# Kernel optimization log

Measured on AMD Instinct MI355X. Metric: run time of the kernel, lower is better.

Reference implementation:

```python
import jax, jax.numpy as jnp
import numpy as np

COST_KEYPOINT = 1.0
COST_GIOU = 1.0


def box_cxcyczwhd_to_xyzxyz(b):
    c, s = b[..., :3], b[..., 3:]
    return jnp.concatenate([c - 0.5 * s, c + 0.5 * s], axis=-1)


def generalized_3d_box_iou(b1, b2):
    # b1: [N,6], b2: [M,6], both xyzxyz. Returns [N,M] GIoU.
    vol1 = jnp.prod(b1[:, 3:] - b1[:, :3], axis=-1)
    vol2 = jnp.prod(b2[:, 3:] - b2[:, :3], axis=-1)
    lt = jnp.maximum(b1[:, None, :3], b2[None, :, :3])
    rb = jnp.minimum(b1[:, None, 3:], b2[None, :, 3:])
    inter = jnp.prod(jnp.maximum(rb - lt, 0.0), axis=-1)
    union = vol1[:, None] + vol2[None, :] - inter
    iou = inter / union
    elt = jnp.minimum(b1[:, None, :3], b2[None, :, :3])
    erb = jnp.maximum(b1[:, None, 3:], b2[None, :, 3:])
    evol = jnp.prod(jnp.maximum(erb - elt, 0.0), axis=-1)
    return iou - (evol - union) / evol


@jax.jit
def compute_cost(pred_keypoints, pred_boxes, tgt_boxes, tgt_keypoints):
    bs, Q = pred_keypoints.shape[:2]
    out_kp = pred_keypoints.reshape(bs * Q, -1)            # [bs*Q, K*3]
    out_boxes = pred_boxes.reshape(bs * Q, 6)
    tgt_b = tgt_boxes.reshape(-1, 6)                        # [T_total, 6]
    tgt_kp = tgt_keypoints.reshape(tgt_b.shape[0], -1)      # [T_total, K*3]
    xyz_min = box_cxcyczwhd_to_xyzxyz(tgt_b)[:, :3]
    K3 = tgt_kp.shape[-1]
    kp = tgt_kp.reshape(-1, K3 // 3, 3)
    # normalize keypoints relative to box min-corner and box size
    dist_kp = ((kp - xyz_min[:, None, :]) / tgt_b[:, None, 3:]).reshape(-1, K3)
    # L1 cdist: [bs*Q, T_total]
    cost_kp = jnp.sum(jnp.abs(out_kp[:, None, :] - dist_kp[None, :, :]), axis=-1)
    cost_giou = -generalized_3d_box_iou(
        box_cxcyczwhd_to_xyzxyz(out_boxes), box_cxcyczwhd_to_xyzxyz(tgt_b))
    C = COST_KEYPOINT * cost_kp + COST_GIOU * cost_giou
    return C.reshape(bs, Q, -1)


def _lap(cost):
    # Jonker-Volgenant shortest-augmenting-path LAP (scipy-style).
    # cost: [n, m] with n <= m. Returns (arange(n), col4row).
    cost = np.asarray(cost, dtype=np.float64)
    n, m = cost.shape
    u = np.zeros(n)
    v = np.zeros(m)
    col4row = np.full(n, -1, np.int64)
    row4col = np.full(m, -1, np.int64)
    for curRow in range(n):
        path = np.full(m, -1, np.int64)
        SR = np.zeros(n, bool)
        SC = np.zeros(m, bool)
        shortest = np.full(m, np.inf)
        minVal = 0.0
        i = curRow
        sink = -1
        while sink == -1:
            SR[i] = True
            idx = np.where(~SC)[0]
            r = minVal + cost[i, idx] - u[i] - v[idx]
            better = r < shortest[idx]
            shortest[idx[better]] = r[better]
            path[idx[better]] = i
            jloc = np.argmin(shortest[idx])
            j = idx[jloc]
            minVal = shortest[j]
            SC[j] = True
            if row4col[j] == -1:
                sink = j
            else:
                i = row4col[j]
        u[curRow] += minVal
        mask = SR.copy()
        mask[curRow] = False
        u[mask] += minVal - shortest[col4row[mask]]
        v[SC] -= minVal - shortest[SC]
        j = sink
        while True:
            i = path[j]
            row4col[j] = i
            col4row[i], j = j, col4row[i]
            if i == curRow:
                break
    return np.arange(n), col4row


def _linear_sum_assignment(cost):
    # cost: [Q, T] with Q >= T; mirrors scipy's transpose handling:
    # returns (row_ind sorted ascending, matching col_ind).
    rows, cols = _lap(cost.T)  # rows = arange(T) targets, cols = query ids
    order = np.argsort(cols)
    return cols[order], rows[order]


def setup_inputs() -> dict:
    key = jax.random.key(0)
    k1, k2, k3, k4, k5, k6 = jax.random.split(key, 6)
    BS, Q, T, K = 16, 300, 50, 17
    pred_keypoints = jax.random.normal(k1, (BS, Q, K * 3), dtype=jnp.float32)
    pred_boxes = jnp.concatenate([
        jax.random.uniform(k2, (BS, Q, 3), dtype=jnp.float32),
        jax.random.uniform(k3, (BS, Q, 3), dtype=jnp.float32) * 0.5 + 0.05,
    ], axis=-1)
    tgt_boxes = jnp.concatenate([
        jax.random.uniform(k4, (BS, T, 3), dtype=jnp.float32),
        jax.random.uniform(k5, (BS, T, 3), dtype=jnp.float32) * 0.5 + 0.05,
    ], axis=-1)
    tgt_keypoints = jax.random.uniform(k6, (BS, T, K * 3), dtype=jnp.float32)
    return {"pred_keypoints": pred_keypoints, "pred_boxes": pred_boxes,
            "tgt_boxes": tgt_boxes, "tgt_keypoints": tgt_keypoints}


def reference(pred_keypoints, pred_boxes, tgt_boxes, tgt_keypoints):
    C = compute_cost(pred_keypoints, pred_boxes, tgt_boxes, tgt_keypoints)
    Cn = np.asarray(C)
    bs, Q, _ = Cn.shape
    T = tgt_boxes.shape[1]
    # per-image block of the column-split cost matrix, as in torch C.split(sizes, -1)
    idx = []
    for b in range(bs):
        i, j = _linear_sum_assignment(Cn[b, :, b * T:(b + 1) * T])
        idx.append(np.stack([i, j]))
    indices = jnp.asarray(np.stack(idx), dtype=jnp.int32)  # [bs, 2, T]
    return C, indices
```

## Files before the change

### kernel.cpp

```cpp
#include <hip/hip_runtime.h>
#include <math.h>

#define BSZ 16
#define NQ 300
#define NT 50
#define K3 51
#define NPRED (BSZ*NQ)
#define NTGT  (BSZ*NT)
#define NC    (NPRED*NTGT)
#define TSTRIDE 301
#define SMEMF 15232

template<int CTRL, int RMASK>
__device__ __forceinline__ double dpp_minstep_f64(double x) {
    long long bb = __double_as_longlong(x);
    int lo = (int)(bb & 0xFFFFFFFFll);
    int hi = (int)(bb >> 32);
    int mlo = __builtin_amdgcn_update_dpp(lo, lo, CTRL, RMASK, 0xF, false);
    int mhi = __builtin_amdgcn_update_dpp(hi, hi, CTRL, RMASK, 0xF, false);
    double other = __longlong_as_double(((long long)mhi << 32) | (long long)(unsigned)mlo);
    return fmin(x, other);
}
__device__ __forceinline__ double wave_min_f64(double x) {
    x = dpp_minstep_f64<0xB1, 0xF>(x);
    x = dpp_minstep_f64<0x4E, 0xF>(x);
    x = dpp_minstep_f64<0x141, 0xF>(x);
    x = dpp_minstep_f64<0x140, 0xF>(x);
    x = dpp_minstep_f64<0x142, 0xA>(x);
    x = dpp_minstep_f64<0x143, 0xC>(x);
    long long bb = __double_as_longlong(x);
    int lo = __builtin_amdgcn_readlane((int)(bb & 0xFFFFFFFFll), 63);
    int hi = __builtin_amdgcn_readlane((int)(bb >> 32), 63);
    return __longlong_as_double(((long long)hi << 32) | (long long)(unsigned)lo);
}
__device__ __forceinline__ double readlane_f64(double x, int lane) {
    long long bb = __double_as_longlong(x);
    int lo = __builtin_amdgcn_readlane((int)(bb & 0xFFFFFFFFll), lane);
    int hi = __builtin_amdgcn_readlane((int)(bb >> 32), lane);
    return __longlong_as_double(((long long)hi << 32) | (long long)(unsigned)lo);
}

__device__ __forceinline__ float giou_cost(
    float plt0, float plt1, float plt2, float prb0, float prb1, float prb2, float pvol,
    float tlt0, float tlt1, float tlt2, float trb0, float trb1, float trb2, float tvol)
{
    float inter = fmaxf(fminf(prb0,trb0) - fmaxf(plt0,tlt0), 0.f);
    inter *= fmaxf(fminf(prb1,trb1) - fmaxf(plt1,tlt1), 0.f);
    inter *= fmaxf(fminf(prb2,trb2) - fmaxf(plt2,tlt2), 0.f);
    float evol = fmaxf(fmaxf(prb0,trb0) - fminf(plt0,tlt0), 0.f);
    evol *= fmaxf(fmaxf(prb1,trb1) - fminf(plt1,tlt1), 0.f);
    evol *= fmaxf(fmaxf(prb2,trb2) - fminf(plt2,tlt2), 0.f);
    float uni = pvol + tvol - inter;
    return inter/uni - (evol - uni)/evol;
}

__global__ __launch_bounds__(1024) void fused_kernel(
    const float* __restrict__ pred_kp, const float* __restrict__ pred_boxes,
    const float* __restrict__ tgt_boxes, const float* __restrict__ tgt_kp,
    float* __restrict__ C, float* __restrict__ out_idx)
{
    __shared__ __align__(16) float smem[SMEMF];
    const int bid = blockIdx.x;
    const int tid = threadIdx.x;

    if (bid >= BSZ) {
        const int cb = bid - BSZ;
        const int pb = cb % 75, tb = cb / 75;
        const int p0 = pb * 64, t0 = tb * 80;
        float* s_dk   = smem;
        float* s_tbox = smem + 4480;
        float* s_pk   = smem + 5440;

        if (tid < 80) {
            const float* tb6 = tgt_boxes + (size_t)(t0 + tid) * 6;
            float c0=tb6[0], c1=tb6[1], c2=tb6[2], s0=tb6[3], s1=tb6[4], s2=tb6[5];
            float l0=c0-0.5f*s0, l1=c1-0.5f*s1, l2=c2-0.5f*s2;
            float r0=c0+0.5f*s0, r1=c1+0.5f*s1, r2=c2+0.5f*s2;
            float* tw = s_tbox + tid*12;
            tw[0]=l0; tw[1]=l1; tw[2]=l2; tw[3]=r0; tw[4]=r1; tw[5]=r2;
            tw[6]=(r0-l0)*(r1-l1)*(r2-l2);
            tw[9]=s0; tw[10]=s1; tw[11]=s2;
        }
        __syncthreads();
        for (int e = tid; e < 80*K3; e += 1024) {
            int t = e / K3; int c = e - t*K3; int d = c % 3;
            float kp = tgt_kp[(size_t)t0*K3 + e];
            s_dk[t*56 + c] = (kp - s_tbox[t*12 + d]) / s_tbox[t*12 + 9 + d];
        }
        for (int e = tid; e < 64*K3; e += 1024)
            s_pk[e] = pred_kp[(size_t)p0*K3 + e];
        __syncthreads();

        const int pl = tid & 63, g = tid >> 6;
        float a[K3];
        #pragma unroll
        for (int c = 0; c < K3; ++c) a[c] = s_pk[pl*K3 + c];
        const int p = p0 + pl;
        const float* pb6 = pred_boxes + (size_t)p * 6;
        float pc0=pb6[0],pc1=pb6[1],pc2=pb6[2],ps0=pb6[3],ps1=pb6[4],ps2=pb6[5];
        float plt0=pc0-0.5f*ps0, plt1=pc1-0.5f*ps1, plt2=pc2-0.5f*ps2;
        float prb0=pc0+0.5f*ps0, prb1=pc1+0.5f*ps1, prb2=pc2+0.5f*ps2;
        float pvol=(prb0-plt0)*(prb1-plt1)*(prb2-plt2);

        #pragma unroll
        for (int k = 0; k < 5; ++k) {
            int tl = g*5 + k;
            const float* bbp = s_dk + tl*56;
            float sum = 0.f;
            #pragma unroll
            for (int c4 = 0; c4 < 12; ++c4) {
                float4 q = *(const float4*)(bbp + 4*c4);
                sum += fabsf(a[4*c4+0] - q.x);
                sum += fabsf(a[4*c4+1] - q.y);
                sum += fabsf(a[4*c4+2] - q.z);
                sum += fabsf(a[4*c4+3] - q.w);
            }
            sum += fabsf(a[48] - bbp[48]);
            sum += fabsf(a[49] - bbp[49]);
            sum += fabsf(a[50] - bbp[50]);
            const float* tw = s_tbox + tl*12;
            float g_ = giou_cost(plt0,plt1,plt2,prb0,prb1,prb2,pvol,
                                 tw[0],tw[1],tw[2],tw[3],tw[4],tw[5],tw[6]);
            C[(size_t)p*NTGT + (t0+tl)] = sum - g_;
        }
        return;
    }

    const int b = bid;
    const int ln = tid & 63, w = tid >> 6;
    const int bq0 = b*NQ, bt0 = b*NT;
    float* tile = smem;

    for (int e = tid; e < NT*K3; e += 1024)
        tile[e] = tgt_kp[(size_t)bt0*K3 + e];
    __syncthreads();

    float dk[K3];
    float tl0=0,tl1=0,tl2=0,tr0=0,tr1=0,tr2=0,tvol=0;
    if (ln < NT) {
        const float* tb6 = tgt_boxes + (size_t)(bt0+ln)*6;
        float c0=tb6[0],c1=tb6[1],c2=tb6[2],s0=tb6[3],s1=tb6[4],s2=tb6[5];
        tl0=c0-0.5f*s0; tl1=c1-0.5f*s1; tl2=c2-0.5f*s2;
        tr0=c0+0.5f*s0; tr1=c1+0.5f*s1; tr2=c2+0.5f*s2;
        tvol=(tr0-tl0)*(tr1-tl1)*(tr2-tl2);
        #pragma unroll
        for (int c = 0; c < K3; ++c) {
            int d = c % 3;
            float L = (d==0)?tl0:((d==1)?tl1:tl2);
            float S = (d==0)?s0:((d==1)?s1:s2);
            dk[c] = (tile[ln*K3 + c] - L) / S;
        }
    }
    __syncthreads();

    for (int p = w; p < NQ; p += 16) {
        const float* prow = pred_kp + (size_t)(bq0+p)*K3;
        const float* pb6  = pred_boxes + (size_t)(bq0+p)*6;
        float pc0=pb6[0],pc1=pb6[1],pc2=pb6[2],ps0=pb6[3],ps1=pb6[4],ps2=pb6[5];
        float plt0=pc0-0.5f*ps0, plt1=pc1-0.5f*ps1, plt2=pc2-0.5f*ps2;
        float prb0=pc0+0.5f*ps0, prb1=pc1+0.5f*ps1, prb2=pc2+0.5f*ps2;
        float pvol=(prb0-plt0)*(prb1-plt1)*(prb2-plt2);
        if (ln < NT) {
            float sum = 0.f;
            #pragma unroll
            for (int c = 0; c < K3; ++c) sum += fabsf(prow[c] - dk[c]);
            float g_ = giou_cost(plt0,plt1,plt2,prb0,prb1,prb2,pvol,
                                 tl0,tl1,tl2,tr0,tr1,tr2,tvol);
            tile[ln*TSTRIDE + p] = sum - g_;
        }
    }
    __syncthreads();

    float* s_rmv = smem + 15072;
    int*   s_rmc = (int*)(smem + 15136);
    for (int r = w; r < NT; r += 16) {
        float bv = __builtin_inff(); int bj = 0x7fffffff;
        #pragma unroll
        for (int s = 0; s < 5; ++s) {
            int j = ln + 64*s;
            if (j < NQ) {
                float cv = tile[r*TSTRIDE + j];
                if (cv < bv || (cv == bv && j < bj)) { bv = cv; bj = j; }
            }
        }
        #pragma unroll
        for (int off = 32; off > 0; off >>= 1) {
            float ov = __shfl_xor(bv, off);
            int   oj = __shfl_xor(bj, off);
            if (ov < bv || (ov == bv && oj < bj)) { bv = ov; bj = oj; }
        }
        if (ln == 0) { s_rmv[r] = bv; s_rmc[r] = bj; }
    }
    __syncthreads();
    if (w != 0) return;

    double u = 0.0;
    int c4r = -1;
    if (ln < NT) u = (double)s_rmv[ln];
    int wantj = (ln < NT) ? s_rmc[ln] : -1;
    for (int r = 0; r < NT; ++r) {
        int j = __builtin_amdgcn_readlane(wantj, r);
        unsigned long long taken = __ballot((ln < NT) && (c4r == j));
        if (taken == 0ull && ln == r) c4r = j;
    }

    double v[5], sh[5];
    int pth[5];
    #pragma unroll
    for (int s = 0; s < 5; ++s) v[s] = 0.0;
    const double DINF = __builtin_inf();

    for (int curRow = 0; curRow < NT; ++curRow) {
        if (__builtin_amdgcn_readlane(c4r, curRow) >= 0) continue;
        #pragma unroll
        for (int s = 0; s < 5; ++s) { sh[s] = DINF; pth[s] = -1; }
        int SCm = (ln < 44) ? 0 : 0x10;
        unsigned long long SRmask = 0ull;
        int i = curRow;
        double minVal = 0.0;
        int sink = -1;

        while (true) {
            SRmask |= (1ull << i);
            float cf[5];
            #pragma unroll
            for (int s = 0; s < 5; ++s) cf[s] = tile[i*TSTRIDE + ln + 64*s];
            double u_i = readlane_f64(u, i);
            double lmin = DINF;
            #pragma unroll
            for (int s = 0; s < 5; ++s) {
                bool open = ((SCm >> s) & 1) == 0;
                double r = ((minVal + (double)cf[s]) - u_i) - v[s];
                bool upd = open && (r < sh[s]);
                sh[s]  = upd ? r : sh[s];
                pth[s] = upd ? i : pth[s];
                lmin = fmin(lmin, open ? sh[s] : DINF);
            }
            double m = wave_min_f64(lmin);
            minVal = m;
            unsigned long long b0 = __ballot((((SCm >> 0) & 1) == 0) && (sh[0] == m));
            unsigned long long b1 = __ballot((((SCm >> 1) & 1) == 0) && (sh[1] == m));
            unsigned long long b2 = __ballot((((SCm >> 2) & 1) == 0) && (sh[2] == m));
            unsigned long long b3 = __ballot((((SCm >> 3) & 1) == 0) && (sh[3] == m));
            unsigned long long b4 = __ballot((((SCm >> 4) & 1) == 0) && (sh[4] == m));
            int jstar;
            if      (b0) jstar =       __builtin_ctzll(b0);
            else if (b1) jstar =  64 + __builtin_ctzll(b1);
            else if (b2) jstar = 128 + __builtin_ctzll(b2);
            else if (b3) jstar = 192 + __builtin_ctzll(b3);
            else         jstar = 256 + __builtin_ctzll(b4);
            if (ln == (jstar & 63)) SCm |= 1 << (jstar >> 6);
            unsigned long long mm = __ballot((ln < NT) && (c4r == jstar));
            if (mm == 0ull) { sink = jstar; break; }
            i = __builtin_ctzll(mm);
        }

        int cg  = (c4r >= 0) ? c4r : 0;
        int gow = cg & 63, gsl = cg >> 6;
        double g0 = __shfl(sh[0], gow);
        double g1 = __shfl(sh[1], gow);
        double g2 = __shfl(sh[2], gow);
        double g3 = __shfl(sh[3], gow);
        double g4 = __shfl(sh[4], gow);
        double gg = g0;
        gg = (gsl == 1) ? g1 : gg;
        gg = (gsl == 2) ? g2 : gg;
        gg = (gsl == 3) ? g3 : gg;
        gg = (gsl == 4) ? g4 : gg;
        bool inSR = (ln < NT) && ((SRmask >> ln) & 1ull);
        double du = (ln == curRow) ? minVal : (minVal - gg);
        u = inSR ? (u + du) : u;
        #pragma unroll
        for (int s = 0; s < 5; ++s) {
            bool closed = ((SCm >> s) & 1) != 0;
            v[s] = closed ? (v[s] - (minVal - sh[s])) : v[s];
        }

        int j = sink;
        while (true) {
            int ow2 = j & 63, sl2 = j >> 6;
            int ps = pth[0];
            ps = (sl2==1) ? pth[1] : ps;
            ps = (sl2==2) ? pth[2] : ps;
            ps = (sl2==3) ? pth[3] : ps;
            ps = (sl2==4) ? pth[4] : ps;
            int ii = __builtin_amdgcn_readlane(ps, ow2);
            int jj = __builtin_amdgcn_readlane(c4r, ii);
            if (ln == ii) c4r = j;
            j = jj;
            if (ii == curRow) break;
        }
    }

    int* smem_i = (int*)smem;
    __threadfence_block();
    if (ln < NT) smem_i[ln] = c4r;
    __threadfence_block();
    int myc = c4r;
    int rank = 0;
    for (int s2 = 0; s2 < NT; ++s2) rank += (smem_i[s2] < myc) ? 1 : 0;
    if (ln < NT) {
        out_idx[b*(2*NT) + rank]      = (float)myc;
        out_idx[b*(2*NT) + NT + rank] = (float)ln;
    }
}

extern "C" void kernel_launch(void* const* d_in, const int* in_sizes, int n_in,
                              void* d_out, int out_size, void* d_ws, size_t ws_size,
                              hipStream_t stream)
{
    const float* pred_kp    = (const float*)d_in[0];
    const float* pred_boxes = (const float*)d_in[1];
    const float* tgt_boxes  = (const float*)d_in[2];
    const float* tgt_kp     = (const float*)d_in[3];
    float* C   = (float*)d_out;
    float* idx = C + NC;
    fused_kernel<<<dim3(BSZ + 750), 1024, 0, stream>>>(
        pred_kp, pred_boxes, tgt_boxes, tgt_kp, C, idx);
}
```

Before: 130.3 us.

## Restructure JV augmentation to track only matched columns plus per-row unmatched minima

Rewrites the shortest-augmenting-path LAP so each lane tracks one matched column slot instead of five column slots per lane. Unmatched columns have v=0, so their reduced cost is given by each row's cheapest unmatched column. Those minima come from a precomputed per-row sorted top-12 list in shared memory, with a full-row rescan when the list runs out. This cuts per-iteration work from five slots and five ballots to one, at the cost of an extra top-k precompute phase and more complex bookkeeping that could diverge on ties.

```diff
diff --git a/kernel.cpp b/kernel.cpp
--- a/kernel.cpp
+++ b/kernel.cpp
@@ -9,7 +9,15 @@
 #define NTGT  (BSZ*NT)
 #define NC    (NPRED*NTGT)
 #define TSTRIDE 301
-#define SMEMF 15232
+#define LT 12
+#define SMEMF 16176
+
+#define OFF_RMV 15072
+#define OFF_RMC 15136
+#define OFF_LV  15200
+#define OFF_LC  15800
+#define OFF_MB  16100
+
 
 template<int CTRL, int RMASK>
 __device__ __forceinline__ double dpp_minstep_f64(double x) {
@@ -38,6 +46,23 @@
     int lo = __builtin_amdgcn_readlane((int)(bb & 0xFFFFFFFFll), lane);
     int hi = __builtin_amdgcn_readlane((int)(bb >> 32), lane);
     return __longlong_as_double(((long long)hi << 32) | (long long)(unsigned)lo);
+}
+__device__ __forceinline__ float readlane_f32(float x, int lane) {
+    return __int_as_float(__builtin_amdgcn_readlane(__float_as_int(x), lane));
+}
+__device__ __forceinline__ double shfl_f64(double x, int lane) {
+    long long bb = __double_as_longlong(x);
+    int lo = __shfl((int)(bb & 0xFFFFFFFFll), lane);
+    int hi = __shfl((int)(bb >> 32), lane);
+    return __longlong_as_double(((long long)hi << 32) | (long long)(unsigned)lo);
+}
+__device__ __forceinline__ void wave_argmin_f32(float &bv, int &bj) {
+    #pragma unroll
+    for (int off = 32; off > 0; off >>= 1) {
+        float ov = __shfl_xor(bv, off);
+        int   oj = __shfl_xor(bj, off);
+        if (ov < bv || (ov == bv && oj < bj)) { bv = ov; bj = oj; }
+    }
 }
 
 __device__ __forceinline__ float giou_cost(
@@ -171,8 +196,12 @@
     }
     __syncthreads();
 
-    float* s_rmv = smem + 15072;
-    int*   s_rmc = (int*)(smem + 15136);
+    float* s_rmv = smem + OFF_RMV;
+    int*   s_rmc = (int*)(smem + OFF_RMC);
+    float* s_lv  = smem + OFF_LV;
+    unsigned short* s_lc = (unsigned short*)(smem + OFF_LC);
+    unsigned char*  s_mb = (unsigned char*)(smem + OFF_MB);
+
     for (int r = w; r < NT; r += 16) {
         float bv = __builtin_inff(); int bj = 0x7fffffff;
         #pragma unroll
@@ -183,14 +212,30 @@
                 if (cv < bv || (cv == bv && j < bj)) { bv = cv; bj = j; }
             }
         }
-        #pragma unroll
-        for (int off = 32; off > 0; off >>= 1) {
-            float ov = __shfl_xor(bv, off);
-            int   oj = __shfl_xor(bj, off);
-            if (ov < bv || (ov == bv && oj < bj)) { bv = ov; bj = oj; }
-        }
+        wave_argmin_f32(bv, bj);
         if (ln == 0) { s_rmv[r] = bv; s_rmc[r] = bj; }
     }
+    for (int r = w; r < NT; r += 16) {
+        float v5[5]; int excl = 0;
+        #pragma unroll
+        for (int s = 0; s < 5; ++s) {
+            int j = ln + 64*s;
+            v5[s] = (j < NQ) ? tile[r*TSTRIDE + j] : __builtin_inff();
+        }
+        for (int k = 0; k < LT; ++k) {
+            float bv = __builtin_inff(); int bj = 0x7fffffff;
+            #pragma unroll
+            for (int s = 0; s < 5; ++s) {
+                int j = ln + 64*s;
+                bool ok = (j < NQ) && !((excl >> s) & 1);
+                if (ok && (v5[s] < bv || (v5[s] == bv && j < bj))) { bv = v5[s]; bj = j; }
+            }
+            wave_argmin_f32(bv, bj);
+            if (ln == 0) { s_lv[r*LT + k] = bv; s_lc[r*LT + k] = (unsigned short)bj; }
+            if (ln == (bj & 63)) excl |= 1 << (bj >> 6);
+        }
+    }
+    for (int e = tid; e < 76; e += 1024) ((int*)(smem + OFF_MB))[e] = 0;
     __syncthreads();
     if (w != 0) return;
 
@@ -203,92 +248,119 @@
         unsigned long long taken = __ballot((ln < NT) && (c4r == j));
         if (taken == 0ull && ln == r) c4r = j;
     }
-
-    double v[5], sh[5];
-    int pth[5];
-    #pragma unroll
-    for (int s = 0; s < 5; ++s) v[s] = 0.0;
+    if (ln < NT && c4r >= 0) s_mb[c4r] = 1;
+    __threadfence_block();
+
+    float buval = __builtin_inff(); int bucol = 0x7fffffff; int buptr = LT;
+    if (ln < NT) {
+        buptr = 0;
+        while (buptr < LT && s_mb[s_lc[ln*LT + buptr]]) ++buptr;
+        if (buptr < LT) { buval = s_lv[ln*LT + buptr]; bucol = s_lc[ln*LT + buptr]; }
+    }
+    {
+        unsigned long long rs = __ballot((ln < NT) && (buptr >= LT));
+        while (rs) {
+            int r = __builtin_ctzll(rs); rs &= rs - 1;
+            float bv = __builtin_inff(); int bj = 0x7fffffff;
+            #pragma unroll
+            for (int s = 0; s < 5; ++s) {
+                int j = ln + 64*s;
+                if (j < NQ && !s_mb[j]) {
+                    float cv = tile[r*TSTRIDE + j];
+                    if (cv < bv || (cv == bv && j < bj)) { bv = cv; bj = j; }
+                }
+            }
+            wave_argmin_f32(bv, bj);
+            if (ln == r) { buval = bv; bucol = bj; }
+        }
+    }
+
+    int nm = 0;
+    int mcol = 0, mrow = 0, s4r = 0;
+    double vs = 0.0;
+    for (int r = 0; r < NT; ++r) {
+        int cr = __builtin_amdgcn_readlane(c4r, r);
+        if (cr >= 0) {
+            if (ln == nm) { mcol = cr; mrow = r; }
+            if (ln == r) s4r = nm;
+            ++nm;
+        }
+    }
+
     const double DINF = __builtin_inf();
 
     for (int curRow = 0; curRow < NT; ++curRow) {
         if (__builtin_amdgcn_readlane(c4r, curRow) >= 0) continue;
-        #pragma unroll
-        for (int s = 0; s < 5; ++s) { sh[s] = DINF; pth[s] = -1; }
-        int SCm = (ln < 44) ? 0 : 0x10;
+        bool open = (ln < nm);
+        double sh = DINF; int pthr = -1;
         unsigned long long SRmask = 0ull;
         int i = curRow;
         double minVal = 0.0;
-        int sink = -1;
-
-        while (true) {
+        double sinkCand = DINF; int sinkCol = -1, sinkRow = -1;
+
+        for (int guard = 0; guard < 512; ++guard) {
             SRmask |= (1ull << i);
-            float cf[5];
-            #pragma unroll
-            for (int s = 0; s < 5; ++s) cf[s] = tile[i*TSTRIDE + ln + 64*s];
-            double u_i = readlane_f64(u, i);
-            double lmin = DINF;
-            #pragma unroll
-            for (int s = 0; s < 5; ++s) {
-                bool open = ((SCm >> s) & 1) == 0;
-                double r = ((minVal + (double)cf[s]) - u_i) - v[s];
-                bool upd = open && (r < sh[s]);
-                sh[s]  = upd ? r : sh[s];
-                pth[s] = upd ? i : pth[s];
-                lmin = fmin(lmin, open ? sh[s] : DINF);
-            }
-            double m = wave_min_f64(lmin);
+            float cf = tile[i*TSTRIDE + mcol];
+            double u_i  = readlane_f64(u, i);
+            float  bu_i = readlane_f32(buval, i);
+            int    buc_i = __builtin_amdgcn_readlane(bucol, i);
+            double rbu = (minVal + (double)bu_i) - u_i;
+            if (rbu < sinkCand) { sinkCand = rbu; sinkCol = buc_i; sinkRow = i; }
+            double rr = ((minVal + (double)cf) - u_i) - vs;
+            bool upd = open && (rr < sh);
+            sh   = upd ? rr : sh;
+            pthr = upd ? i : pthr;
+            double m = wave_min_f64(open ? sh : DINF);
+            if (sinkCand < m) { minVal = sinkCand; break; }
             minVal = m;
-            unsigned long long b0 = __ballot((((SCm >> 0) & 1) == 0) && (sh[0] == m));
-            unsigned long long b1 = __ballot((((SCm >> 1) & 1) == 0) && (sh[1] == m));
-            unsigned long long b2 = __ballot((((SCm >> 2) & 1) == 0) && (sh[2] == m));
-            unsigned long long b3 = __ballot((((SCm >> 3) & 1) == 0) && (sh[3] == m));
-            unsigned long long b4 = __ballot((((SCm >> 4) & 1) == 0) && (sh[4] == m));
-            int jstar;
-            if      (b0) jstar =       __builtin_ctzll(b0);
-            else if (b1) jstar =  64 + __builtin_ctzll(b1);
-            else if (b2) jstar = 128 + __builtin_ctzll(b2);
-            else if (b3) jstar = 192 + __builtin_ctzll(b3);
-            else         jstar = 256 + __builtin_ctzll(b4);
-            if (ln == (jstar & 63)) SCm |= 1 << (jstar >> 6);
-            unsigned long long mm = __ballot((ln < NT) && (c4r == jstar));
-            if (mm == 0ull) { sink = jstar; break; }
-            i = __builtin_ctzll(mm);
-        }
-
-        int cg  = (c4r >= 0) ? c4r : 0;
-        int gow = cg & 63, gsl = cg >> 6;
-        double g0 = __shfl(sh[0], gow);
-        double g1 = __shfl(sh[1], gow);
-        double g2 = __shfl(sh[2], gow);
-        double g3 = __shfl(sh[3], gow);
-        double g4 = __shfl(sh[4], gow);
-        double gg = g0;
-        gg = (gsl == 1) ? g1 : gg;
-        gg = (gsl == 2) ? g2 : gg;
-        gg = (gsl == 3) ? g3 : gg;
-        gg = (gsl == 4) ? g4 : gg;
+            unsigned long long bb = __ballot(open && (sh == m));
+            int slot = __builtin_ctzll(bb);
+            if (ln == slot) open = false;
+            i = __builtin_amdgcn_readlane(mrow, slot);
+        }
+
+        bool valid = (ln < nm);
+        double gg = shfl_f64(sh, (c4r >= 0) ? s4r : 0);
         bool inSR = (ln < NT) && ((SRmask >> ln) & 1ull);
         double du = (ln == curRow) ? minVal : (minVal - gg);
         u = inSR ? (u + du) : u;
-        #pragma unroll
-        for (int s = 0; s < 5; ++s) {
-            bool closed = ((SCm >> s) & 1) != 0;
-            v[s] = closed ? (v[s] - (minVal - sh[s])) : v[s];
-        }
-
-        int j = sink;
-        while (true) {
-            int ow2 = j & 63, sl2 = j >> 6;
-            int ps = pth[0];
-            ps = (sl2==1) ? pth[1] : ps;
-            ps = (sl2==2) ? pth[2] : ps;
-            ps = (sl2==3) ? pth[3] : ps;
-            ps = (sl2==4) ? pth[4] : ps;
-            int ii = __builtin_amdgcn_readlane(ps, ow2);
-            int jj = __builtin_amdgcn_readlane(c4r, ii);
-            if (ln == ii) c4r = j;
-            j = jj;
+        bool closedSlot = valid && !open;
+        vs = closedSlot ? (vs - (minVal - sh)) : vs;
+
+        int jcol = sinkCol, jslot = nm, ii = sinkRow;
+        if (ln == nm) { mcol = sinkCol; vs = 0.0; }
+        for (int guard = 0; guard < 64; ++guard) {
+            int oldc = __builtin_amdgcn_readlane(c4r, ii);
+            int olds = __builtin_amdgcn_readlane(s4r, ii);
+            if (ln == jslot) mrow = ii;
+            if (ln == ii) { c4r = jcol; s4r = jslot; }
             if (ii == curRow) break;
+            jcol = oldc; jslot = olds;
+            ii = __builtin_amdgcn_readlane(pthr, jslot);
+        }
+        ++nm;
+        if (ln == 0) s_mb[sinkCol] = 1;
+        __threadfence_block();
+
+        bool need = (ln < NT) && (bucol == sinkCol);
+        if (need) {
+            while (buptr < LT && s_mb[s_lc[ln*LT + buptr]]) ++buptr;
+            if (buptr < LT) { buval = s_lv[ln*LT + buptr]; bucol = s_lc[ln*LT + buptr]; need = false; }
+        }
+        unsigned long long rs = __ballot(need);
+        while (rs) {
+            int r = __builtin_ctzll(rs); rs &= rs - 1;
+            float bv = __builtin_inff(); int bj = 0x7fffffff;
+            #pragma unroll
+            for (int s = 0; s < 5; ++s) {
+                int j = ln + 64*s;
+                if (j < NQ && !s_mb[j]) {
+                    float cv = tile[r*TSTRIDE + j];
+                    if (cv < bv || (cv == bv && j < bj)) { bv = cv; bj = j; }
+                }
+            }
+            wave_argmin_f32(bv, bj);
+            if (ln == r) { buval = bv; bucol = bj; }
         }
     }
 
```

After: 168.2 us. 29.1% more time.
